# Optimization experiments

Measured on AMD Instinct MI355X. Metric: run time of the kernel, lower is better.

Reference implementation:

```python
import jax, jax.numpy as jnp
import numpy as np

NUM_HEADS = 8
EPS = 1e-5


def setup_inputs() -> dict:
    key = jax.random.key(0)
    ks = jax.random.split(key, 12)
    B, S, D = 16384, 12, 512
    s = 1.0 / np.sqrt(D)
    return {
        "x": jax.random.normal(ks[0], (B, S, D), dtype=jnp.float32),
        "Wq": jax.random.uniform(ks[1], (D, D), jnp.float32, -s, s),
        "bq": jax.random.uniform(ks[2], (D,), jnp.float32, -s, s),
        "Wk": jax.random.uniform(ks[3], (D, D), jnp.float32, -s, s),
        "bk": jax.random.uniform(ks[4], (D,), jnp.float32, -s, s),
        "Wv": jax.random.uniform(ks[5], (D, D), jnp.float32, -s, s),
        "bv": jax.random.uniform(ks[6], (D,), jnp.float32, -s, s),
        "adj_bias": jnp.zeros((NUM_HEADS, S, S), dtype=jnp.float32),
        "Wo": jax.random.uniform(ks[7], (D, D), jnp.float32, -s, s),
        "bo": jax.random.uniform(ks[8], (D,), jnp.float32, -s, s),
        "gamma": jnp.ones((D,), dtype=jnp.float32),
        "beta": jnp.zeros((D,), dtype=jnp.float32),
    }


def reference(x, Wq, bq, Wk, bk, Wv, bv, adj_bias, Wo, bo, gamma, beta):
    B, S, D = x.shape
    H = NUM_HEADS
    hd = D // H
    # QKV projections -> (B, H, S, hd)
    def proj(W, b):
        return (jnp.einsum('bsd,de->bse', x, W) + b).reshape(B, S, H, hd).transpose(0, 2, 1, 3)
    q = proj(Wq, bq)
    k = proj(Wk, bk)
    v = proj(Wv, bv)
    # scores with learned adjacency bias: (B, H, S, S)
    scores = jnp.einsum('bhsd,bhtd->bhst', q, k) / np.sqrt(hd).astype(np.float32)
    scores = scores + adj_bias[None, :, :S, :S]
    attn = jax.nn.softmax(scores, axis=-1)  # dropout is identity in eval mode
    out = jnp.einsum('bhst,bhtd->bhsd', attn, v)
    out = out.transpose(0, 2, 1, 3).reshape(B, S, D)
    out = jnp.einsum('bsd,de->bse', out, Wo) + bo
    # residual (in_dim == out_dim) + LayerNorm
    y = out + x
    mu = jnp.mean(y, axis=-1, keepdims=True)
    var = jnp.mean(jnp.square(y - mu), axis=-1, keepdims=True)
    return (y - mu) * jax.lax.rsqrt(var + EPS) * gamma + beta
```

## Files before the change

kernel.cpp:

```cpp
#include <hip/hip_runtime.h>
#include <hip/hip_bf16.h>

#define D_DIM 512
#define S_LEN 12
#define H_NUM 8
#define WMAT 262144

#define G_B1 8
#define ROWS1 96
#define THREADS1 768
#define X_OFF   0
#define Q_OFF   98304
#define K_OFF   110592
#define V_OFF   122880
#define P_OFF   135168
#define SMEM1   142848

#define G_B2 8
#define ROWS2 96
#define THREADS2 512
#define AST_OFF 0
#define RED_OFF 98304
#define MU_OFF  104832
#define SMEM2   105600


typedef __attribute__((ext_vector_type(8))) short bf16x8;
typedef __attribute__((ext_vector_type(4))) float f32x4;

__device__ __forceinline__ unsigned short f2bf(float f) {
    union { float f; unsigned u; } c; c.f = f;
    unsigned r = c.u + 0x7fffu + ((c.u >> 16) & 1u);
    return (unsigned short)(r >> 16);
}
__device__ __forceinline__ float bf2f(unsigned short u) {
    union { unsigned u; float f; } c; c.u = ((unsigned)u) << 16;
    return c.f;
}
__device__ __forceinline__ int xswc(int row, int col) {
    return row * 512 + (((col >> 3) ^ (row & 7)) << 3) + (col & 7);
}
__device__ __forceinline__ int qsw(int row, int col) {
    return row * 64 + (((col >> 3) ^ (row & 7)) << 3) + (col & 7);
}

__global__ void prep_weights(const float* __restrict__ Wq, const float* __restrict__ Wk,
                             const float* __restrict__ Wv, const float* __restrict__ Wo,
                             unsigned short* __restrict__ wt) {
    int idx = blockIdx.x * 256 + threadIdx.x;
    int mat = idx >> 18;
    int rem = idx & (WMAT - 1);
    int e = rem >> 9, d = rem & 511;
    const float* W = (mat == 0) ? Wq : (mat == 1) ? Wk : (mat == 2) ? Wv : Wo;
    wt[idx] = f2bf(W[d * D_DIM + e]);
}

__global__ __launch_bounds__(THREADS1, 3) void qkv_attn(
    const float* __restrict__ x, const unsigned short* __restrict__ wt,
    const float* __restrict__ bq, const float* __restrict__ bk, const float* __restrict__ bv,
    const float* __restrict__ adj, unsigned short* __restrict__ aout)
{
    extern __shared__ char smem[];
    unsigned short* Xh = (unsigned short*)(smem + X_OFF);
    unsigned short* Qh = (unsigned short*)(smem + Q_OFF);
    unsigned short* Kh = (unsigned short*)(smem + K_OFF);
    unsigned short* Vh = (unsigned short*)(smem + V_OFF);
    float* Pl = (float*)(smem + P_OFF);

    const int tid  = threadIdx.x;
    const int lane = tid & 63;
    const int w    = tid >> 6;
    const int lr   = lane & 15;
    const int lg   = lane >> 4;
    const int lr12 = (lr < 12) ? lr : 11;
    const size_t row0 = (size_t)blockIdx.x * ROWS1;

    #pragma unroll
    for (int it = 0; it < 16; ++it) {
        int idx = it * THREADS1 + tid;
        int r = idx >> 7, col = (idx & 127) << 2;
        float4 v = *(const float4*)(x + (row0 + r) * (size_t)D_DIM + col);
        ushort4 pk;
        pk.x = f2bf(v.x); pk.y = f2bf(v.y); pk.z = f2bf(v.z); pk.w = f2bf(v.w);
        *(ushort4*)(Xh + xswc(r, col)) = pk;
    }
    __syncthreads();

    const int mat  = w >> 2;
    const int colt = w & 3;
    const int colh = colt * 16 + lr;
    const float* bsel = (mat == 0) ? bq : (mat == 1) ? bk : bv;
    unsigned short* T = (mat == 0) ? Qh : (mat == 1) ? Kh : Vh;
    const int rb = w * S_LEN;

    #pragma unroll 1
    for (int h = 0; h < H_NUM; ++h) {
        f32x4 acc[6];
        #pragma unroll
        for (int mt = 0; mt < 6; ++mt) acc[mt] = (f32x4){0.f, 0.f, 0.f, 0.f};

        const unsigned short* bAp = wt + (size_t)mat * WMAT + (h * 64 + colh) * D_DIM + lg * 8;
        bf16x8 bc = *(const bf16x8*)(bAp);
        #pragma unroll
        for (int ks = 0; ks < 16; ++ks) {
            bf16x8 bn;
            if (ks < 15) bn = *(const bf16x8*)(bAp + (ks + 1) * 32);
            #pragma unroll
            for (int mt = 0; mt < 6; ++mt) {
                bf16x8 af = *(const bf16x8*)(Xh + xswc(mt * 16 + lr, ks * 32 + lg * 8));
                acc[mt] = __builtin_amdgcn_mfma_f32_16x16x32_bf16(af, bc, acc[mt], 0, 0, 0);
            }
            if (ks < 15) bc = bn;
        }
        {
            float bias = bsel[h * 64 + colh];
            #pragma unroll
            for (int mt = 0; mt < 6; ++mt)
                #pragma unroll
                for (int j = 0; j < 4; ++j)
                    T[qsw(mt * 16 + lg * 4 + j, colh)] = f2bf(acc[mt][j] + bias);
        }
        __syncthreads();

        if (w < 8) {
            f32x4 sacc = (f32x4){0.f, 0.f, 0.f, 0.f};
            #pragma unroll
            for (int k2 = 0; k2 < 2; ++k2) {
                bf16x8 ak = *(const bf16x8*)(Kh + qsw(rb + lr12, k2 * 32 + lg * 8));
                bf16x8 aq = *(const bf16x8*)(Qh + qsw(rb + lr12, k2 * 32 + lg * 8));
                sacc = __builtin_amdgcn_mfma_f32_16x16x32_bf16(ak, aq, sacc, 0, 0, 0);
            }
            float ab4[4] = {0.f, 0.f, 0.f, 0.f};
            if (lg < 3 && lr < 12) {
                float4 t4 = *(const float4*)(adj + (h * S_LEN + lr) * S_LEN + lg * 4);
                ab4[0] = t4.x; ab4[1] = t4.y; ab4[2] = t4.z; ab4[3] = t4.w;
            }
            float sc[4], e4[4];
            float m = -1e30f;
            #pragma unroll
            for (int j = 0; j < 4; ++j) {
                int t = lg * 4 + j;
                sc[j] = (t < 12) ? (sacc[j] * 0.125f + ab4[j]) : -1e30f;
                m = fmaxf(m, sc[j]);
            }
            m = fmaxf(m, __shfl_xor(m, 16));
            m = fmaxf(m, __shfl_xor(m, 32));
            float ssum = 0.f;
            #pragma unroll
            for (int j = 0; j < 4; ++j) { e4[j] = __expf(sc[j] - m); ssum += e4[j]; }
            ssum += __shfl_xor(ssum, 16);
            ssum += __shfl_xor(ssum, 32);
            float inv = 1.f / ssum;
            float* Pw = Pl + w * 240;
            if (lr < 12 && lg < 3) {
                f32x4 pvec = (f32x4){e4[0] * inv, e4[1] * inv, e4[2] * inv, e4[3] * inv};
                *(f32x4*)(Pw + lr * 20 + lg * 4) = pvec;
            }
            float vv[12];
            #pragma unroll
            for (int t = 0; t < 12; ++t) vv[t] = bf2f(Vh[qsw(rb + t, lane)]);
            #pragma unroll
            for (int ss = 0; ss < 12; ++ss) {
                f32x4 pa = *(const f32x4*)(Pw + ss * 20);
                f32x4 pb = *(const f32x4*)(Pw + ss * 20 + 4);
                f32x4 pc = *(const f32x4*)(Pw + ss * 20 + 8);
                float o = 0.f;
                #pragma unroll
                for (int t = 0; t < 4; ++t) o += pa[t] * vv[t];
                #pragma unroll
                for (int t = 0; t < 4; ++t) o += pb[t] * vv[4 + t];
                #pragma unroll
                for (int t = 0; t < 4; ++t) o += pc[t] * vv[8 + t];
                aout[(row0 + rb + ss) * 1024 + h * 64 + lane] = f2bf(o);
            }
        }
        __syncthreads();
    }
}

__global__ __launch_bounds__(THREADS2, 2) void oproj_ln(
    const float* __restrict__ x, const unsigned short* __restrict__ wt,
    const float* __restrict__ bo, const float* __restrict__ gamma,
    const float* __restrict__ beta, float* __restrict__ out)
{
    extern __shared__ char smem[];
    unsigned short* Ast = (unsigned short*)(smem + AST_OFF);
    float* red   = (float*)(smem + RED_OFF);
    float* musig = (float*)(smem + MU_OFF);

    const int tid  = threadIdx.x;
    const int lane = tid & 63;
    const int w    = tid >> 6;
    const int lr   = lane & 15;
    const int lg   = lane >> 4;
    const size_t row0 = (size_t)blockIdx.x * ROWS2;
    const unsigned short* abase = (const unsigned short*)out;

    #pragma unroll
    for (int it = 0; it < 12; ++it) {
        int idx = it * THREADS2 + tid;
        int r = idx >> 6, c8 = (idx & 63) << 3;
        uint4 v = *(const uint4*)(abase + (row0 + r) * 1024 + c8);
        *(uint4*)(Ast + xswc(r, c8)) = v;
    }
    __syncthreads();

    f32x4 Y[6][4];
    #pragma unroll
    for (int mt = 0; mt < 6; ++mt)
        #pragma unroll
        for (int nt = 0; nt < 4; ++nt) Y[mt][nt] = (f32x4){0.f, 0.f, 0.f, 0.f};

    const unsigned short* obase = wt + (size_t)3 * WMAT + (w * 64 + lr) * D_DIM;
    #pragma unroll 1
    for (int ks = 0; ks < 16; ++ks) {
        bf16x8 afr[6];
        #pragma unroll
        for (int mt = 0; mt < 6; ++mt)
            afr[mt] = *(const bf16x8*)(Ast + xswc(mt * 16 + lr, ks * 32 + lg * 8));
        #pragma unroll
        for (int nt = 0; nt < 4; ++nt) {
            bf16x8 bfr = *(const bf16x8*)(obase + nt * 16 * D_DIM + ks * 32 + lg * 8);
            #pragma unroll
            for (int mt = 0; mt < 6; ++mt)
                Y[mt][nt] = __builtin_amdgcn_mfma_f32_16x16x32_bf16(afr[mt], bfr, Y[mt][nt], 0, 0, 0);
        }
    }

    float bo4[4], gm4[4], bt4[4];
    int cols[4];
    #pragma unroll
    for (int nt = 0; nt < 4; ++nt) {
        cols[nt] = w * 64 + nt * 16 + lr;
        bo4[nt] = bo[cols[nt]]; gm4[nt] = gamma[cols[nt]]; bt4[nt] = beta[cols[nt]];
    }
    #pragma unroll
    for (int mt = 0; mt < 6; ++mt)
        #pragma unroll
        for (int j = 0; j < 4; ++j) {
            int rowl = mt * 16 + lg * 4 + j;
            const float* xrow = x + (row0 + rowl) * (size_t)D_DIM;
            float ps = 0.f, pq = 0.f;
            #pragma unroll
            for (int nt = 0; nt < 4; ++nt) {
                float y = Y[mt][nt][j] + bo4[nt] + xrow[cols[nt]];
                Y[mt][nt][j] = y;
                ps += y; pq += y * y;
            }
            ps += __shfl_xor(ps, 1); pq += __shfl_xor(pq, 1);
            ps += __shfl_xor(ps, 2); pq += __shfl_xor(pq, 2);
            ps += __shfl_xor(ps, 4); pq += __shfl_xor(pq, 4);
            ps += __shfl_xor(ps, 8); pq += __shfl_xor(pq, 8);
            if (lr == 0) { red[rowl * 17 + w * 2] = ps; red[rowl * 17 + w * 2 + 1] = pq; }
        }
    __syncthreads();
    if (tid < ROWS2) {
        float s = 0.f, q = 0.f;
        #pragma unroll
        for (int w8 = 0; w8 < 8; ++w8) { s += red[tid * 17 + w8 * 2]; q += red[tid * 17 + w8 * 2 + 1]; }
        float mu = s * (1.f / 512.f);
        float var = q * (1.f / 512.f) - mu * mu;
        musig[tid * 2] = mu;
        musig[tid * 2 + 1] = rsqrtf(var + 1e-5f);
    }
    __syncthreads();
    #pragma unroll
    for (int mt = 0; mt < 6; ++mt)
        #pragma unroll
        for (int j = 0; j < 4; ++j) {
            int rowl = mt * 16 + lg * 4 + j;
            float mu = musig[rowl * 2], rs = musig[rowl * 2 + 1];
            float* orow = out + (row0 + rowl) * (size_t)D_DIM;
            #pragma unroll
            for (int nt = 0; nt < 4; ++nt)
                orow[cols[nt]] = (Y[mt][nt][j] - mu) * rs * gm4[nt] + bt4[nt];
        }
}

extern "C" void kernel_launch(void* const* d_in, const int* in_sizes, int n_in,
                              void* d_out, int out_size, void* d_ws, size_t ws_size,
                              hipStream_t stream) {
    (void)in_sizes; (void)n_in; (void)out_size; (void)ws_size;
    const float* x     = (const float*)d_in[0];
    const float* Wq    = (const float*)d_in[1];
    const float* bq    = (const float*)d_in[2];
    const float* Wk    = (const float*)d_in[3];
    const float* bk    = (const float*)d_in[4];
    const float* Wv    = (const float*)d_in[5];
    const float* bv    = (const float*)d_in[6];
    const float* adj   = (const float*)d_in[7];
    const float* Wo    = (const float*)d_in[8];
    const float* bo    = (const float*)d_in[9];
    const float* gamma = (const float*)d_in[10];
    const float* beta  = (const float*)d_in[11];
    unsigned short* wt = (unsigned short*)d_ws;

    prep_weights<<<4096, 256, 0, stream>>>(Wq, Wk, Wv, Wo, wt);
    qkv_attn<<<16384 / G_B1, THREADS1, SMEM1, stream>>>(
        x, wt, bq, bk, bv, adj, (unsigned short*)d_out);
    oproj_ln<<<16384 / G_B2, THREADS2, SMEM2, stream>>>(
        x, wt, bo, gamma, beta, (float*)d_out);
}
```

Measured before the change: 943.4 us.

## Compute two heads per QKV projection pass and shuffle softmax probabilities

Each warp now computes 32 output columns for one of two heads per iteration, so every A fragment read from LDS feeds two MFMAs. The head loop drops from 8 to 4 passes, and Q/K buffers double to hold two heads. V for the second head is written after the first head's attention finishes. The softmax probabilities no longer go through an LDS scratch buffer; they are broadcast with lane shuffles during the PV product. The cost is more LDS, which may lower occupancy below the launch-bound target of 3 blocks, more accumulator registers, and extra barriers.

```diff
diff --git a/kernel.cpp b/kernel.cpp
--- a/kernel.cpp
+++ b/kernel.cpp
@@ -9,12 +9,12 @@
 #define G_B1 8
 #define ROWS1 96
 #define THREADS1 768
+#define TBLK    6144
 #define X_OFF   0
 #define Q_OFF   98304
-#define K_OFF   110592
-#define V_OFF   122880
-#define P_OFF   135168
-#define SMEM1   142848
+#define K_OFF   122880
+#define V_OFF   147456
+#define SMEM1   159744
 
 #define G_B2 8
 #define ROWS2 96
@@ -65,7 +65,6 @@
     unsigned short* Qh = (unsigned short*)(smem + Q_OFF);
     unsigned short* Kh = (unsigned short*)(smem + K_OFF);
     unsigned short* Vh = (unsigned short*)(smem + V_OFF);
-    float* Pl = (float*)(smem + P_OFF);
 
     const int tid  = threadIdx.x;
     const int lane = tid & 63;
@@ -86,92 +85,176 @@
     }
     __syncthreads();
 
-    const int mat  = w >> 2;
-    const int colt = w & 3;
-    const int colh = colt * 16 + lr;
+    const int mat = w >> 2;
+    const int hh  = (w >> 1) & 1;
+    const int c0  = (w & 1) * 32;
     const float* bsel = (mat == 0) ? bq : (mat == 1) ? bk : bv;
-    unsigned short* T = (mat == 0) ? Qh : (mat == 1) ? Kh : Vh;
     const int rb = w * S_LEN;
 
     #pragma unroll 1
-    for (int h = 0; h < H_NUM; ++h) {
-        f32x4 acc[6];
-        #pragma unroll
-        for (int mt = 0; mt < 6; ++mt) acc[mt] = (f32x4){0.f, 0.f, 0.f, 0.f};
-
-        const unsigned short* bAp = wt + (size_t)mat * WMAT + (h * 64 + colh) * D_DIM + lg * 8;
-        bf16x8 bc = *(const bf16x8*)(bAp);
+    for (int hg = 0; hg < 4; ++hg) {
+        const int h = hg * 2 + hh;
+        f32x4 acc[6][2];
+        #pragma unroll
+        for (int mt = 0; mt < 6; ++mt) {
+            acc[mt][0] = (f32x4){0.f, 0.f, 0.f, 0.f};
+            acc[mt][1] = (f32x4){0.f, 0.f, 0.f, 0.f};
+        }
+        const unsigned short* bp0 = wt + (size_t)mat * WMAT + (h * 64 + c0 + lr) * D_DIM + lg * 8;
+        const unsigned short* bp1 = bp0 + 16 * D_DIM;
         #pragma unroll
         for (int ks = 0; ks < 16; ++ks) {
-            bf16x8 bn;
-            if (ks < 15) bn = *(const bf16x8*)(bAp + (ks + 1) * 32);
+            bf16x8 b0 = *(const bf16x8*)(bp0 + ks * 32);
+            bf16x8 b1 = *(const bf16x8*)(bp1 + ks * 32);
             #pragma unroll
             for (int mt = 0; mt < 6; ++mt) {
                 bf16x8 af = *(const bf16x8*)(Xh + xswc(mt * 16 + lr, ks * 32 + lg * 8));
-                acc[mt] = __builtin_amdgcn_mfma_f32_16x16x32_bf16(af, bc, acc[mt], 0, 0, 0);
-            }
-            if (ks < 15) bc = bn;
+                acc[mt][0] = __builtin_amdgcn_mfma_f32_16x16x32_bf16(af, b0, acc[mt][0], 0, 0, 0);
+                acc[mt][1] = __builtin_amdgcn_mfma_f32_16x16x32_bf16(af, b1, acc[mt][1], 0, 0, 0);
+            }
         }
         {
-            float bias = bsel[h * 64 + colh];
-            #pragma unroll
-            for (int mt = 0; mt < 6; ++mt)
-                #pragma unroll
-                for (int j = 0; j < 4; ++j)
-                    T[qsw(mt * 16 + lg * 4 + j, colh)] = f2bf(acc[mt][j] + bias);
+            float bias0 = bsel[h * 64 + c0 + lr];
+            float bias1 = bsel[h * 64 + c0 + 16 + lr];
+            if (mat < 2) {
+                unsigned short* T = ((mat == 0) ? Qh : Kh) + hh * TBLK;
+                #pragma unroll
+                for (int mt = 0; mt < 6; ++mt)
+                    #pragma unroll
+                    for (int j = 0; j < 4; ++j) {
+                        int rowl = mt * 16 + lg * 4 + j;
+                        T[qsw(rowl, c0 + lr)]      = f2bf(acc[mt][0][j] + bias0);
+                        T[qsw(rowl, c0 + 16 + lr)] = f2bf(acc[mt][1][j] + bias1);
+                    }
+            } else if (hh == 0) {
+                #pragma unroll
+                for (int mt = 0; mt < 6; ++mt)
+                    #pragma unroll
+                    for (int j = 0; j < 4; ++j) {
+                        int rowl = mt * 16 + lg * 4 + j;
+                        Vh[qsw(rowl, c0 + lr)]      = f2bf(acc[mt][0][j] + bias0);
+                        Vh[qsw(rowl, c0 + 16 + lr)] = f2bf(acc[mt][1][j] + bias1);
+                    }
+            }
         }
         __syncthreads();
 
         if (w < 8) {
+            const int ha = hg * 2;
+            const unsigned short* Qb = Qh;
+            const unsigned short* Kb = Kh;
             f32x4 sacc = (f32x4){0.f, 0.f, 0.f, 0.f};
             #pragma unroll
             for (int k2 = 0; k2 < 2; ++k2) {
-                bf16x8 ak = *(const bf16x8*)(Kh + qsw(rb + lr12, k2 * 32 + lg * 8));
-                bf16x8 aq = *(const bf16x8*)(Qh + qsw(rb + lr12, k2 * 32 + lg * 8));
+                bf16x8 ak = *(const bf16x8*)(Kb + qsw(rb + lr12, k2 * 32 + lg * 8));
+                bf16x8 aq = *(const bf16x8*)(Qb + qsw(rb + lr12, k2 * 32 + lg * 8));
                 sacc = __builtin_amdgcn_mfma_f32_16x16x32_bf16(ak, aq, sacc, 0, 0, 0);
             }
             float ab4[4] = {0.f, 0.f, 0.f, 0.f};
             if (lg < 3 && lr < 12) {
-                float4 t4 = *(const float4*)(adj + (h * S_LEN + lr) * S_LEN + lg * 4);
+                float4 t4 = *(const float4*)(adj + (ha * S_LEN + lr) * S_LEN + lg * 4);
                 ab4[0] = t4.x; ab4[1] = t4.y; ab4[2] = t4.z; ab4[3] = t4.w;
             }
-            float sc[4], e4[4];
-            float m = -1e30f;
-            #pragma unroll
-            for (int j = 0; j < 4; ++j) {
-                int t = lg * 4 + j;
-                sc[j] = (t < 12) ? (sacc[j] * 0.125f + ab4[j]) : -1e30f;
-                m = fmaxf(m, sc[j]);
-            }
-            m = fmaxf(m, __shfl_xor(m, 16));
-            m = fmaxf(m, __shfl_xor(m, 32));
-            float ssum = 0.f;
-            #pragma unroll
-            for (int j = 0; j < 4; ++j) { e4[j] = __expf(sc[j] - m); ssum += e4[j]; }
-            ssum += __shfl_xor(ssum, 16);
-            ssum += __shfl_xor(ssum, 32);
-            float inv = 1.f / ssum;
-            float* Pw = Pl + w * 240;
-            if (lr < 12 && lg < 3) {
-                f32x4 pvec = (f32x4){e4[0] * inv, e4[1] * inv, e4[2] * inv, e4[3] * inv};
-                *(f32x4*)(Pw + lr * 20 + lg * 4) = pvec;
+            float e4n[4];
+            {
+                float sc[4];
+                float m = -1e30f;
+                #pragma unroll
+                for (int j = 0; j < 4; ++j) {
+                    int tt = lg * 4 + j;
+                    sc[j] = (tt < 12) ? (sacc[j] * 0.125f + ab4[j]) : -1e30f;
+                    m = fmaxf(m, sc[j]);
+                }
+                m = fmaxf(m, __shfl_xor(m, 16));
+                m = fmaxf(m, __shfl_xor(m, 32));
+                float ssum = 0.f;
+                #pragma unroll
+                for (int j = 0; j < 4; ++j) { e4n[j] = __expf(sc[j] - m); ssum += e4n[j]; }
+                ssum += __shfl_xor(ssum, 16);
+                ssum += __shfl_xor(ssum, 32);
+                float inv = 1.f / ssum;
+                #pragma unroll
+                for (int j = 0; j < 4; ++j) e4n[j] *= inv;
             }
             float vv[12];
             #pragma unroll
             for (int t = 0; t < 12; ++t) vv[t] = bf2f(Vh[qsw(rb + t, lane)]);
             #pragma unroll
             for (int ss = 0; ss < 12; ++ss) {
-                f32x4 pa = *(const f32x4*)(Pw + ss * 20);
-                f32x4 pb = *(const f32x4*)(Pw + ss * 20 + 4);
-                f32x4 pc = *(const f32x4*)(Pw + ss * 20 + 8);
                 float o = 0.f;
                 #pragma unroll
-                for (int t = 0; t < 4; ++t) o += pa[t] * vv[t];
-                #pragma unroll
-                for (int t = 0; t < 4; ++t) o += pb[t] * vv[4 + t];
-                #pragma unroll
-                for (int t = 0; t < 4; ++t) o += pc[t] * vv[8 + t];
-                aout[(row0 + rb + ss) * 1024 + h * 64 + lane] = f2bf(o);
+                for (int t = 0; t < 12; ++t) {
+                    float pt = __shfl(e4n[t & 3], ss + ((t >> 2) << 4));
+                    o += pt * vv[t];
+                }
+                aout[(row0 + rb + ss) * 1024 + ha * 64 + lane] = f2bf(o);
+            }
+        }
+        __syncthreads();
+
+        if (mat == 2 && hh == 1) {
+            float bias0 = bsel[h * 64 + c0 + lr];
+            float bias1 = bsel[h * 64 + c0 + 16 + lr];
+            #pragma unroll
+            for (int mt = 0; mt < 6; ++mt)
+                #pragma unroll
+                for (int j = 0; j < 4; ++j) {
+                    int rowl = mt * 16 + lg * 4 + j;
+                    Vh[qsw(rowl, c0 + lr)]      = f2bf(acc[mt][0][j] + bias0);
+                    Vh[qsw(rowl, c0 + 16 + lr)] = f2bf(acc[mt][1][j] + bias1);
+                }
+        }
+        __syncthreads();
+
+        if (w < 8) {
+            const int ha = hg * 2 + 1;
+            const unsigned short* Qb = Qh + TBLK;
+            const unsigned short* Kb = Kh + TBLK;
+            f32x4 sacc = (f32x4){0.f, 0.f, 0.f, 0.f};
+            #pragma unroll
+            for (int k2 = 0; k2 < 2; ++k2) {
+                bf16x8 ak = *(const bf16x8*)(Kb + qsw(rb + lr12, k2 * 32 + lg * 8));
+                bf16x8 aq = *(const bf16x8*)(Qb + qsw(rb + lr12, k2 * 32 + lg * 8));
+                sacc = __builtin_amdgcn_mfma_f32_16x16x32_bf16(ak, aq, sacc, 0, 0, 0);
+            }
+            float ab4[4] = {0.f, 0.f, 0.f, 0.f};
+            if (lg < 3 && lr < 12) {
+                float4 t4 = *(const float4*)(adj + (ha * S_LEN + lr) * S_LEN + lg * 4);
+                ab4[0] = t4.x; ab4[1] = t4.y; ab4[2] = t4.z; ab4[3] = t4.w;
+            }
+            float e4n[4];
+            {
+                float sc[4];
+                float m = -1e30f;
+                #pragma unroll
+                for (int j = 0; j < 4; ++j) {
+                    int tt = lg * 4 + j;
+                    sc[j] = (tt < 12) ? (sacc[j] * 0.125f + ab4[j]) : -1e30f;
+                    m = fmaxf(m, sc[j]);
+                }
+                m = fmaxf(m, __shfl_xor(m, 16));
+                m = fmaxf(m, __shfl_xor(m, 32));
+                float ssum = 0.f;
+                #pragma unroll
+                for (int j = 0; j < 4; ++j) { e4n[j] = __expf(sc[j] - m); ssum += e4n[j]; }
+                ssum += __shfl_xor(ssum, 16);
+                ssum += __shfl_xor(ssum, 32);
+                float inv = 1.f / ssum;
+                #pragma unroll
+                for (int j = 0; j < 4; ++j) e4n[j] *= inv;
+            }
+            float vv[12];
+            #pragma unroll
+            for (int t = 0; t < 12; ++t) vv[t] = bf2f(Vh[qsw(rb + t, lane)]);
+            #pragma unroll
+            for (int ss = 0; ss < 12; ++ss) {
+                float o = 0.f;
+                #pragma unroll
+                for (int t = 0; t < 12; ++t) {
+                    float pt = __shfl(e4n[t & 3], ss + ((t >> 2) << 4));
+                    o += pt * vv[t];
+                }
+                aout[(row0 + rb + ss) * 1024 + ha * 64 + lane] = f2bf(o);
             }
         }
         __syncthreads();
```

Measured after the change: 1.724 ms. 82.8% more time.

## Switch QKV projection to 32x32x16 MFMA with asymmetric row split across waves

Applied to the files above, without the earlier changes.

The QKV projection stage now uses 32x32x16 bf16 MFMA tiles instead of 16x16x32. The 12 waves split into 6 that compute one 32-row tile and 6 that compute two 32-row tiles, all sharing the same weight fragment loads. This is meant to cut LDS and global weight traffic per MFMA and raise matrix-core throughput. The cost is an unbalanced workload: half the waves do twice the MFMA work, and the weight prefetch pipelining is dropped.

```diff
diff --git a/kernel.cpp b/kernel.cpp
--- a/kernel.cpp
+++ b/kernel.cpp
@@ -27,6 +27,7 @@
 
 typedef __attribute__((ext_vector_type(8))) short bf16x8;
 typedef __attribute__((ext_vector_type(4))) float f32x4;
+typedef __attribute__((ext_vector_type(16))) float f32x16;
 
 __device__ __forceinline__ unsigned short f2bf(float f) {
     union { float f; unsigned u; } c; c.f = f;
@@ -86,39 +87,54 @@
     }
     __syncthreads();
 
-    const int mat  = w >> 2;
-    const int colt = w & 3;
-    const int colh = colt * 16 + lr;
+    const int p    = (w < 6) ? w : (w - 6);
+    const int role = (w < 6) ? 0 : 1;
+    const int mat  = p >> 1;
+    const int colb = (p & 1) * 32;
+    const int c32  = lane & 31;
+    const int k8   = (lane >> 5) * 8;
+    const int ro   = (lane >> 5) * 4;
     const float* bsel = (mat == 0) ? bq : (mat == 1) ? bk : bv;
     unsigned short* T = (mat == 0) ? Qh : (mat == 1) ? Kh : Vh;
     const int rb = w * S_LEN;
 
     #pragma unroll 1
     for (int h = 0; h < H_NUM; ++h) {
-        f32x4 acc[6];
-        #pragma unroll
-        for (int mt = 0; mt < 6; ++mt) acc[mt] = (f32x4){0.f, 0.f, 0.f, 0.f};
-
-        const unsigned short* bAp = wt + (size_t)mat * WMAT + (h * 64 + colh) * D_DIM + lg * 8;
-        bf16x8 bc = *(const bf16x8*)(bAp);
-        #pragma unroll
-        for (int ks = 0; ks < 16; ++ks) {
-            bf16x8 bn;
-            if (ks < 15) bn = *(const bf16x8*)(bAp + (ks + 1) * 32);
-            #pragma unroll
-            for (int mt = 0; mt < 6; ++mt) {
-                bf16x8 af = *(const bf16x8*)(Xh + xswc(mt * 16 + lr, ks * 32 + lg * 8));
-                acc[mt] = __builtin_amdgcn_mfma_f32_16x16x32_bf16(af, bc, acc[mt], 0, 0, 0);
-            }
-            if (ks < 15) bc = bn;
-        }
-        {
-            float bias = bsel[h * 64 + colh];
-            #pragma unroll
-            for (int mt = 0; mt < 6; ++mt)
-                #pragma unroll
-                for (int j = 0; j < 4; ++j)
-                    T[qsw(mt * 16 + lg * 4 + j, colh)] = f2bf(acc[mt][j] + bias);
+        const unsigned short* bp = wt + (size_t)mat * WMAT + (h * 64 + colb + c32) * D_DIM + k8;
+        float bias = bsel[h * 64 + colb + c32];
+        if (role == 0) {
+            f32x16 acc;
+            #pragma unroll
+            for (int i = 0; i < 16; ++i) acc[i] = 0.f;
+            #pragma unroll
+            for (int ks = 0; ks < 32; ++ks) {
+                bf16x8 b = *(const bf16x8*)(bp + ks * 16);
+                bf16x8 af = *(const bf16x8*)(Xh + xswc(c32, ks * 16 + k8));
+                acc = __builtin_amdgcn_mfma_f32_32x32x16_bf16(af, b, acc, 0, 0, 0);
+            }
+            #pragma unroll
+            for (int reg = 0; reg < 16; ++reg) {
+                int row = (reg & 3) + 8 * (reg >> 2) + ro;
+                T[qsw(row, colb + c32)] = f2bf(acc[reg] + bias);
+            }
+        } else {
+            f32x16 a1, a2;
+            #pragma unroll
+            for (int i = 0; i < 16; ++i) { a1[i] = 0.f; a2[i] = 0.f; }
+            #pragma unroll
+            for (int ks = 0; ks < 32; ++ks) {
+                bf16x8 b = *(const bf16x8*)(bp + ks * 16);
+                bf16x8 af1 = *(const bf16x8*)(Xh + xswc(32 + c32, ks * 16 + k8));
+                bf16x8 af2 = *(const bf16x8*)(Xh + xswc(64 + c32, ks * 16 + k8));
+                a1 = __builtin_amdgcn_mfma_f32_32x32x16_bf16(af1, b, a1, 0, 0, 0);
+                a2 = __builtin_amdgcn_mfma_f32_32x32x16_bf16(af2, b, a2, 0, 0, 0);
+            }
+            #pragma unroll
+            for (int reg = 0; reg < 16; ++reg) {
+                int row = (reg & 3) + 8 * (reg >> 2) + ro;
+                T[qsw(32 + row, colb + c32)] = f2bf(a1[reg] + bias);
+                T[qsw(64 + row, colb + c32)] = f2bf(a2[reg] + bias);
+            }
         }
         __syncthreads();
 
```

Result: slower. 1.275 ms (+35.1%).

## Fuse output projection and LayerNorm into the QKV-attention kernel

Applied to the files above, without the earlier changes.

Merges the separate output-projection/LayerNorm kernel into the attention kernel so one block of 96 rows handles both stages. The attention output still goes through global memory (the output buffer), but the block reads it back right away, likely from cache, and the second launch is gone. The O-projection is re-tiled for 12 waves (3 row groups × 4 column groups of 128), and shared memory is reused for the reduction scratch. In exchange, the fused kernel is bound to the first kernel's occupancy and launch bounds, and bias/gamma/beta are loaded per element instead of being hoisted.

```diff
diff --git a/kernel.cpp b/kernel.cpp
--- a/kernel.cpp
+++ b/kernel.cpp
@@ -6,23 +6,15 @@
 #define H_NUM 8
 #define WMAT 262144
 
-#define G_B1 8
-#define ROWS1 96
-#define THREADS1 768
+#define G_B 8
+#define ROWS 96
+#define THREADS 768
 #define X_OFF   0
 #define Q_OFF   98304
 #define K_OFF   110592
 #define V_OFF   122880
 #define P_OFF   135168
-#define SMEM1   142848
-
-#define G_B2 8
-#define ROWS2 96
-#define THREADS2 512
-#define AST_OFF 0
-#define RED_OFF 98304
-#define MU_OFF  104832
-#define SMEM2   105600
+#define SMEM    142848
 
 
 typedef __attribute__((ext_vector_type(8))) short bf16x8;
@@ -55,17 +47,23 @@
     wt[idx] = f2bf(W[d * D_DIM + e]);
 }
 
-__global__ __launch_bounds__(THREADS1, 3) void qkv_attn(
+__global__ __launch_bounds__(THREADS, 3) void fused_all(
     const float* __restrict__ x, const unsigned short* __restrict__ wt,
     const float* __restrict__ bq, const float* __restrict__ bk, const float* __restrict__ bv,
-    const float* __restrict__ adj, unsigned short* __restrict__ aout)
+    const float* __restrict__ adj, const float* __restrict__ bo,
+    const float* __restrict__ gamma, const float* __restrict__ beta,
+    float* __restrict__ out)
 {
     extern __shared__ char smem[];
     unsigned short* Xh = (unsigned short*)(smem + X_OFF);
     unsigned short* Qh = (unsigned short*)(smem + Q_OFF);
     unsigned short* Kh = (unsigned short*)(smem + K_OFF);
     unsigned short* Vh = (unsigned short*)(smem + V_OFF);
-    float* Pl = (float*)(smem + P_OFF);
+    float* Pl    = (float*)(smem + P_OFF);
+    float* red   = (float*)(smem + P_OFF);
+    float* musig = (float*)(smem + P_OFF + 3456);
+
+    unsigned short* aout = (unsigned short*)out;
 
     const int tid  = threadIdx.x;
     const int lane = tid & 63;
@@ -73,11 +71,11 @@
     const int lr   = lane & 15;
     const int lg   = lane >> 4;
     const int lr12 = (lr < 12) ? lr : 11;
-    const size_t row0 = (size_t)blockIdx.x * ROWS1;
+    const size_t row0 = (size_t)blockIdx.x * ROWS;
 
     #pragma unroll
     for (int it = 0; it < 16; ++it) {
-        int idx = it * THREADS1 + tid;
+        int idx = it * THREADS + tid;
         int r = idx >> 7, col = (idx & 127) << 2;
         float4 v = *(const float4*)(x + (row0 + r) * (size_t)D_DIM + col);
         ushort4 pk;
@@ -176,74 +174,48 @@
         }
         __syncthreads();
     }
-}
-
-__global__ __launch_bounds__(THREADS2, 2) void oproj_ln(
-    const float* __restrict__ x, const unsigned short* __restrict__ wt,
-    const float* __restrict__ bo, const float* __restrict__ gamma,
-    const float* __restrict__ beta, float* __restrict__ out)
-{
-    extern __shared__ char smem[];
-    unsigned short* Ast = (unsigned short*)(smem + AST_OFF);
-    float* red   = (float*)(smem + RED_OFF);
-    float* musig = (float*)(smem + MU_OFF);
-
-    const int tid  = threadIdx.x;
-    const int lane = tid & 63;
-    const int w    = tid >> 6;
-    const int lr   = lane & 15;
-    const int lg   = lane >> 4;
-    const size_t row0 = (size_t)blockIdx.x * ROWS2;
-    const unsigned short* abase = (const unsigned short*)out;
-
-    #pragma unroll
-    for (int it = 0; it < 12; ++it) {
-        int idx = it * THREADS2 + tid;
+
+    #pragma unroll
+    for (int it = 0; it < 8; ++it) {
+        int idx = it * THREADS + tid;
         int r = idx >> 6, c8 = (idx & 63) << 3;
-        uint4 v = *(const uint4*)(abase + (row0 + r) * 1024 + c8);
-        *(uint4*)(Ast + xswc(r, c8)) = v;
-    }
-    __syncthreads();
-
-    f32x4 Y[6][4];
-    #pragma unroll
-    for (int mt = 0; mt < 6; ++mt)
-        #pragma unroll
-        for (int nt = 0; nt < 4; ++nt) Y[mt][nt] = (f32x4){0.f, 0.f, 0.f, 0.f};
-
-    const unsigned short* obase = wt + (size_t)3 * WMAT + (w * 64 + lr) * D_DIM;
+        uint4 v = *(const uint4*)(aout + (row0 + r) * 1024 + c8);
+        *(uint4*)(Xh + xswc(r, c8)) = v;
+    }
+    __syncthreads();
+
+    const int rg = w >> 2;
+    const int cg = w & 3;
+    f32x4 Y[2][8];
+    #pragma unroll
+    for (int mt = 0; mt < 2; ++mt)
+        #pragma unroll
+        for (int nt = 0; nt < 8; ++nt) Y[mt][nt] = (f32x4){0.f, 0.f, 0.f, 0.f};
+
+    const unsigned short* obase = wt + (size_t)3 * WMAT + (cg * 128 + lr) * D_DIM;
     #pragma unroll 1
     for (int ks = 0; ks < 16; ++ks) {
-        bf16x8 afr[6];
-        #pragma unroll
-        for (int mt = 0; mt < 6; ++mt)
-            afr[mt] = *(const bf16x8*)(Ast + xswc(mt * 16 + lr, ks * 32 + lg * 8));
-        #pragma unroll
-        for (int nt = 0; nt < 4; ++nt) {
+        bf16x8 af0 = *(const bf16x8*)(Xh + xswc(rg * 32 + lr,      ks * 32 + lg * 8));
+        bf16x8 af1 = *(const bf16x8*)(Xh + xswc(rg * 32 + 16 + lr, ks * 32 + lg * 8));
+        #pragma unroll
+        for (int nt = 0; nt < 8; ++nt) {
             bf16x8 bfr = *(const bf16x8*)(obase + nt * 16 * D_DIM + ks * 32 + lg * 8);
-            #pragma unroll
-            for (int mt = 0; mt < 6; ++mt)
-                Y[mt][nt] = __builtin_amdgcn_mfma_f32_16x16x32_bf16(afr[mt], bfr, Y[mt][nt], 0, 0, 0);
-        }
-    }
-
-    float bo4[4], gm4[4], bt4[4];
-    int cols[4];
-    #pragma unroll
-    for (int nt = 0; nt < 4; ++nt) {
-        cols[nt] = w * 64 + nt * 16 + lr;
-        bo4[nt] = bo[cols[nt]]; gm4[nt] = gamma[cols[nt]]; bt4[nt] = beta[cols[nt]];
-    }
-    #pragma unroll
-    for (int mt = 0; mt < 6; ++mt)
+            Y[0][nt] = __builtin_amdgcn_mfma_f32_16x16x32_bf16(af0, bfr, Y[0][nt], 0, 0, 0);
+            Y[1][nt] = __builtin_amdgcn_mfma_f32_16x16x32_bf16(af1, bfr, Y[1][nt], 0, 0, 0);
+        }
+    }
+
+    #pragma unroll
+    for (int mt = 0; mt < 2; ++mt)
         #pragma unroll
         for (int j = 0; j < 4; ++j) {
-            int rowl = mt * 16 + lg * 4 + j;
+            int rowl = rg * 32 + mt * 16 + lg * 4 + j;
             const float* xrow = x + (row0 + rowl) * (size_t)D_DIM;
             float ps = 0.f, pq = 0.f;
             #pragma unroll
-            for (int nt = 0; nt < 4; ++nt) {
-                float y = Y[mt][nt][j] + bo4[nt] + xrow[cols[nt]];
+            for (int nt = 0; nt < 8; ++nt) {
+                int c = cg * 128 + nt * 16 + lr;
+                float y = Y[mt][nt][j] + bo[c] + xrow[c];
                 Y[mt][nt][j] = y;
                 ps += y; pq += y * y;
             }
@@ -251,29 +223,32 @@
             ps += __shfl_xor(ps, 2); pq += __shfl_xor(pq, 2);
             ps += __shfl_xor(ps, 4); pq += __shfl_xor(pq, 4);
             ps += __shfl_xor(ps, 8); pq += __shfl_xor(pq, 8);
-            if (lr == 0) { red[rowl * 17 + w * 2] = ps; red[rowl * 17 + w * 2 + 1] = pq; }
-        }
-    __syncthreads();
-    if (tid < ROWS2) {
+            if (lr == 0) { red[rowl * 9 + cg * 2] = ps; red[rowl * 9 + cg * 2 + 1] = pq; }
+        }
+    __syncthreads();
+    if (tid < ROWS) {
         float s = 0.f, q = 0.f;
         #pragma unroll
-        for (int w8 = 0; w8 < 8; ++w8) { s += red[tid * 17 + w8 * 2]; q += red[tid * 17 + w8 * 2 + 1]; }
+        for (int c4 = 0; c4 < 4; ++c4) { s += red[tid * 9 + c4 * 2]; q += red[tid * 9 + c4 * 2 + 1]; }
         float mu = s * (1.f / 512.f);
         float var = q * (1.f / 512.f) - mu * mu;
         musig[tid * 2] = mu;
         musig[tid * 2 + 1] = rsqrtf(var + 1e-5f);
     }
     __syncthreads();
-    #pragma unroll
-    for (int mt = 0; mt < 6; ++mt)
+
+    #pragma unroll
+    for (int mt = 0; mt < 2; ++mt)
         #pragma unroll
         for (int j = 0; j < 4; ++j) {
-            int rowl = mt * 16 + lg * 4 + j;
+            int rowl = rg * 32 + mt * 16 + lg * 4 + j;
             float mu = musig[rowl * 2], rs = musig[rowl * 2 + 1];
             float* orow = out + (row0 + rowl) * (size_t)D_DIM;
             #pragma unroll
-            for (int nt = 0; nt < 4; ++nt)
-                orow[cols[nt]] = (Y[mt][nt][j] - mu) * rs * gm4[nt] + bt4[nt];
+            for (int nt = 0; nt < 8; ++nt) {
+                int c = cg * 128 + nt * 16 + lr;
+                orow[c] = (Y[mt][nt][j] - mu) * rs * gamma[c] + beta[c];
+            }
         }
 }
 
@@ -296,8 +271,6 @@
     unsigned short* wt = (unsigned short*)d_ws;
 
     prep_weights<<<4096, 256, 0, stream>>>(Wq, Wk, Wv, Wo, wt);
-    qkv_attn<<<16384 / G_B1, THREADS1, SMEM1, stream>>>(
-        x, wt, bq, bk, bv, adj, (unsigned short*)d_out);
-    oproj_ln<<<16384 / G_B2, THREADS2, SMEM2, stream>>>(
-        x, wt, bo, gamma, beta, (float*)d_out);
-}
+    fused_all<<<16384 / G_B, THREADS, SMEM, stream>>>(
+        x, wt, bq, bk, bv, adj, bo, gamma, beta, (float*)d_out);
+}
```

Measured after the change: 1.051 ms. 11.4% more time.
